# Optimization experiments

Hardware: AMD Instinct MI355X
Metric: run time of the kernel (lower is better)

## Reference

```python
import jax, jax.numpy as jnp
import numpy as np

B, LQ, LM, D, H = 2, 2048, 2048, 1024, 16
DH = D // H  # 64

def setup_inputs() -> dict:
    key = jax.random.key(0)
    ks = jax.random.split(key, 11)
    s = 0.02
    return {
        "query": jax.random.normal(ks[0], (B, LQ, D), jnp.float32),
        "memory": jax.random.normal(ks[1], (B, LM, D), jnp.float32),
        "memory_bias": jax.random.normal(ks[2], (B, LM), jnp.float32),
        "Wq": jax.random.normal(ks[3], (D, D), jnp.float32) * s,
        "bq": jnp.zeros((D,), jnp.float32),
        "Wk": jax.random.normal(ks[4], (D, D), jnp.float32) * s,
        "bk": jnp.zeros((D,), jnp.float32),
        "Wv": jax.random.normal(ks[5], (D, D), jnp.float32) * s,
        "bv": jnp.zeros((D,), jnp.float32),
        "Wo": jax.random.normal(ks[6], (D, D), jnp.float32) * s,
        "bo": jnp.zeros((D,), jnp.float32),
    }

def reference(query, memory, memory_bias, Wq, bq, Wk, bk, Wv, bv, Wo, bo):
    # QKV projections, split into heads: [B, L, H, DH]
    q = (query @ Wq + bq).reshape(B, LQ, H, DH)
    k = (memory @ Wk + bk).reshape(B, LM, H, DH)
    v = (memory @ Wv + bv).reshape(B, LM, H, DH)
    q = q * (DH ** -0.5)
    # logits: [B, H, Lq, Lk] (matches torch.einsum('btnh,bfnh->bnft', k, q))
    logits = jnp.einsum("bfnh,btnh->bnft", q, k)
    logits = logits + memory_bias[:, None, None, :]  # bias [B, Lm] -> [B,1,1,Lk]
    weights = jax.nn.softmax(logits, axis=-1)
    # dropout omitted (eval / rate 0 for correctness baseline)
    attn = jnp.einsum("bnft,btnh->bfnh", weights, v).reshape(B, LQ, D)
    return attn @ Wo + bo  # [B, Lq, output_depth]
```

## Files before the change

### kernel.cpp

```cpp
#include <hip/hip_runtime.h>
#include <hip/hip_bf16.h>
#include <math.h>


typedef __bf16 bf16;
typedef __bf16 bf16x4 __attribute__((ext_vector_type(4)));
typedef __bf16 bf16x8 __attribute__((ext_vector_type(8)));
typedef float f32x4 __attribute__((ext_vector_type(4)));

#define MFMA16(a, b, c) __builtin_amdgcn_mfma_f32_16x16x32_bf16((a), (b), (c), 0, 0, 0)

__device__ inline float exp2_hw(float x) {
    float r; asm("v_exp_f32 %0, %1" : "=v"(r) : "v"(x)); return r;
}

__device__ inline void gload_lds16(const bf16* g, bf16* l) {
    __builtin_amdgcn_global_load_lds(
        (const __attribute__((address_space(1))) void*)g,
        (__attribute__((address_space(3))) void*)l, 16, 0, 0);
}

__global__ __launch_bounds__(256) void cvt_kernel(
    const float* __restrict__ X0, const float* __restrict__ X1,
    bf16* __restrict__ Y0, bf16* __restrict__ Y1)
{
    const float* X = blockIdx.y ? X1 : X0;
    bf16* Y = blockIdx.y ? Y1 : Y0;
    const size_t i = ((size_t)blockIdx.x * 256 + threadIdx.x) * 8;
    float4 f0 = *(const float4*)&X[i];
    float4 f1 = *(const float4*)&X[i + 4];
    bf16x8 h;
    h[0] = (bf16)f0.x; h[1] = (bf16)f0.y; h[2] = (bf16)f0.z; h[3] = (bf16)f0.w;
    h[4] = (bf16)f1.x; h[5] = (bf16)f1.y; h[6] = (bf16)f1.z; h[7] = (bf16)f1.w;
    *(bf16x8*)&Y[i] = h;
}

__global__ __launch_bounds__(256) void transpose_cvt_kernel(
    const float* __restrict__ W0, const float* __restrict__ W1,
    const float* __restrict__ W2, const float* __restrict__ W3,
    bf16* __restrict__ T0, bf16* __restrict__ T1,
    bf16* __restrict__ T2, bf16* __restrict__ T3)
{
    __shared__ float Ls[64][65];
    const float* W; bf16* T;
    switch (blockIdx.z) {
        case 0:  W = W0; T = T0; break;
        case 1:  W = W1; T = T1; break;
        case 2:  W = W2; T = T2; break;
        default: W = W3; T = T3; break;
    }
    const int t = threadIdx.x;
    const int n0 = blockIdx.x * 64, k0 = blockIdx.y * 64;
    const int g = t >> 4, c = (t & 15) * 4;

    #pragma unroll
    for (int p = 0; p < 4; ++p) {
        const int row = p * 16 + g;
        float4 f = *(const float4*)&W[(size_t)(k0 + row) * 1024 + n0 + c];
        Ls[row][c + 0] = f.x; Ls[row][c + 1] = f.y;
        Ls[row][c + 2] = f.z; Ls[row][c + 3] = f.w;
    }
    __syncthreads();
    #pragma unroll
    for (int p = 0; p < 4; ++p) {
        const int n = p * 16 + g;
        bf16x4 h;
        h[0] = (bf16)Ls[c + 0][n]; h[1] = (bf16)Ls[c + 1][n];
        h[2] = (bf16)Ls[c + 2][n]; h[3] = (bf16)Ls[c + 3][n];
        *(bf16x4*)&T[(size_t)(n0 + n) * 1024 + k0 + c] = h;
    }
}

template <typename TO>
__global__ __launch_bounds__(256) void gemm_kernel(
    const bf16* __restrict__ A, const bf16* __restrict__ WT,
    const float* __restrict__ bias, TO* __restrict__ out,
    float alpha, int mode)
{
    __shared__ __align__(16) bf16 As[2][128 * 64];
    __shared__ __align__(16) bf16 Bs[2][64 * 64];

    const int fid = blockIdx.x + (blockIdx.y << 4);
    const int swz = (fid & 7) * 64 + (fid >> 3);
    const int n0 = (swz & 15) * 64;
    const int m0 = (swz >> 4) * 128;

    const int tid = threadIdx.x;
    const int w = tid >> 6, lane = tid & 63;
    const int lr = lane & 15, lg = lane >> 4;
    const int wm = (w >> 1) * 64, wn = (w & 1) * 32;

    const int arow0 = w * 32 + (lane >> 3);
    const int brow0 = w * 16 + (lane >> 3);
    const int sch = lane & 7;

    f32x4 acc[4][2] = {};

    auto stageG = [&](int kt, int bi) {
        #pragma unroll
        for (int p = 0; p < 4; ++p) {
            const int row = arow0 + p * 8;
            const int xc = ((sch ^ (row & 7)) << 3);
            gload_lds16(&A[(size_t)(m0 + row) * 1024 + kt + xc],
                        &As[bi][row * 64 + sch * 8]);
        }
        #pragma unroll
        for (int p = 0; p < 2; ++p) {
            const int row = brow0 + p * 8;
            const int xc = ((sch ^ (row & 7)) << 3);
            gload_lds16(&WT[(size_t)(n0 + row) * 1024 + kt + xc],
                        &Bs[bi][row * 64 + sch * 8]);
        }
    };

    stageG(0, 0);
    __syncthreads();

    int cur = 0;
    #pragma unroll 1
    for (int t = 0; t < 16; ++t) {
        if (t < 15) stageG((t + 1) * 64, cur ^ 1);

        #pragma unroll
        for (int ks = 0; ks < 2; ++ks) {
            const int c = (((ks * 4 + lg) ^ (lr & 7)) << 3);
            bf16x8 af[4], bfv[2];
            #pragma unroll
            for (int mt = 0; mt < 4; ++mt)
                af[mt] = *(const bf16x8*)&As[cur][(wm + mt * 16 + lr) * 64 + c];
            #pragma unroll
            for (int nt = 0; nt < 2; ++nt)
                bfv[nt] = *(const bf16x8*)&Bs[cur][(wn + nt * 16 + lr) * 64 + c];
            #pragma unroll
            for (int nt = 0; nt < 2; ++nt)
                #pragma unroll
                for (int mt = 0; mt < 4; ++mt)
                    acc[mt][nt] = MFMA16(af[mt], bfv[nt], acc[mt][nt]);
        }
        __syncthreads();
        cur ^= 1;
    }

    #pragma unroll
    for (int nt = 0; nt < 2; ++nt) {
        const int n = n0 + wn + nt * 16 + lr;
        const float bv = bias[n];
        #pragma unroll
        for (int mt = 0; mt < 4; ++mt) {
            #pragma unroll
            for (int i = 0; i < 4; ++i) {
                const int m = m0 + wm + mt * 16 + lg * 4 + i;
                const float v = (acc[mt][nt][i] + bv) * alpha;
                if (mode == 0) {
                    out[(size_t)m * 1024 + n] = (TO)v;
                } else {
                    const int b = m >> 11, t2 = m & 2047;
                    out[((size_t)(b << 10) + n) * 2048 + t2] = (TO)v;
                }
            }
        }
    }
}

__global__ __launch_bounds__(256) void gemm_kv_kernel(
    const bf16* __restrict__ A, const bf16* __restrict__ WTk,
    const bf16* __restrict__ WTv, const float* __restrict__ bk,
    const float* __restrict__ bv, bf16* __restrict__ Kout,
    bf16* __restrict__ Vtout)
{
    __shared__ __align__(16) bf16 As[2][128 * 64];
    __shared__ __align__(16) bf16 Bk[2][64 * 64];
    __shared__ __align__(16) bf16 Bv[2][64 * 64];

    const int fid = blockIdx.x + (blockIdx.y << 4);
    const int swz = (fid & 7) * 64 + (fid >> 3);
    const int n0 = (swz & 15) * 64;
    const int m0 = (swz >> 4) * 128;

    const int tid = threadIdx.x;
    const int w = tid >> 6, lane = tid & 63;
    const int lr = lane & 15, lg = lane >> 4;
    const int wm = (w >> 1) * 64, wn = (w & 1) * 32;

    const int arow0 = w * 32 + (lane >> 3);
    const int brow0 = w * 16 + (lane >> 3);
    const int sch = lane & 7;

    f32x4 accK[4][2] = {}, accV[4][2] = {};

    auto stageG = [&](int kt, int bi) {
        #pragma unroll
        for (int p = 0; p < 4; ++p) {
            const int row = arow0 + p * 8;
            const int xc = ((sch ^ (row & 7)) << 3);
            gload_lds16(&A[(size_t)(m0 + row) * 1024 + kt + xc],
                        &As[bi][row * 64 + sch * 8]);
        }
        #pragma unroll
        for (int p = 0; p < 2; ++p) {
            const int row = brow0 + p * 8;
            const int xc = ((sch ^ (row & 7)) << 3);
            gload_lds16(&WTk[(size_t)(n0 + row) * 1024 + kt + xc],
                        &Bk[bi][row * 64 + sch * 8]);
            gload_lds16(&WTv[(size_t)(n0 + row) * 1024 + kt + xc],
                        &Bv[bi][row * 64 + sch * 8]);
        }
    };

    stageG(0, 0);
    __syncthreads();

    int cur = 0;
    #pragma unroll 1
    for (int t = 0; t < 16; ++t) {
        if (t < 15) stageG((t + 1) * 64, cur ^ 1);

        #pragma unroll
        for (int ks = 0; ks < 2; ++ks) {
            const int c = (((ks * 4 + lg) ^ (lr & 7)) << 3);
            bf16x8 af[4], bkf[2], bvf[2];
            #pragma unroll
            for (int mt = 0; mt < 4; ++mt)
                af[mt] = *(const bf16x8*)&As[cur][(wm + mt * 16 + lr) * 64 + c];
            #pragma unroll
            for (int nt = 0; nt < 2; ++nt) {
                bkf[nt] = *(const bf16x8*)&Bk[cur][(wn + nt * 16 + lr) * 64 + c];
                bvf[nt] = *(const bf16x8*)&Bv[cur][(wn + nt * 16 + lr) * 64 + c];
            }
            #pragma unroll
            for (int nt = 0; nt < 2; ++nt)
                #pragma unroll
                for (int mt = 0; mt < 4; ++mt) {
                    accK[mt][nt] = MFMA16(af[mt], bkf[nt], accK[mt][nt]);
                    accV[mt][nt] = MFMA16(af[mt], bvf[nt], accV[mt][nt]);
                }
        }
        __syncthreads();
        cur ^= 1;
    }

    #pragma unroll
    for (int nt = 0; nt < 2; ++nt) {
        const int n = n0 + wn + nt * 16 + lr;
        const float bkv = bk[n], bvv = bv[n];
        #pragma unroll
        for (int mt = 0; mt < 4; ++mt) {
            #pragma unroll
            for (int i = 0; i < 4; ++i) {
                const int m = m0 + wm + mt * 16 + lg * 4 + i;
                Kout[(size_t)m * 1024 + n] = (bf16)(accK[mt][nt][i] + bkv);
                const int b = m >> 11, t2 = m & 2047;
                Vtout[((size_t)(b << 10) + n) * 2048 + t2] = (bf16)(accV[mt][nt][i] + bvv);
            }
        }
    }
}

__global__ __launch_bounds__(512, 4) void attn_kernel(
    const bf16* __restrict__ Q, const bf16* __restrict__ K,
    const bf16* __restrict__ Vt, const float* __restrict__ mbias,
    bf16* __restrict__ Oout)
{
    __shared__ __align__(16) bf16 Kbuf[4][4096];
    __shared__ __align__(16) bf16 Vbuf[4][4096];

    const int tid = threadIdx.x;
    const int w = tid >> 6, lane = tid & 63;
    const int lr = lane & 15, lg = lane >> 4;

    const int fid = blockIdx.x + (blockIdx.y << 4) + (blockIdx.z << 8);
    const int swz = (fid & 7) * 64 + (fid >> 3);
    const int qt = swz & 15, head = (swz >> 4) & 15, b = swz >> 8;
    const int qrow = qt * 128 + w * 16;

    const size_t qo = (size_t)(b * 2048 + qrow + lr) * 1024 + head * 64;
    bf16x8 qf[2];
    qf[0] = *(const bf16x8*)&Q[qo + lg * 8];
    qf[1] = *(const bf16x8*)&Q[qo + 32 + lg * 8];

    const bf16* Kb = K + (size_t)b * 2048 * 1024 + head * 64;
    const bf16* Vb = Vt + ((size_t)b * 1024 + head * 64) * 2048;
    const float* biasb = mbias + b * 2048;

    float m_run = -INFINITY;
    f32x4 of[4] = {};
    f32x4 ofl = {};

    bf16x8 ones8;
    #pragma unroll
    for (int j = 0; j < 8; ++j) ones8[j] = (bf16)1.0f;

    const int chunk = w * 64 + lane;
    const int R = chunk >> 3, cc = chunk & 7;
    const int cs = cc ^ (R & 7);
    const int piR = ((R & 16) << 1) | ((R & 12) << 1) | ((R & 32) >> 3) | (R & 3);
    auto stage = [&](int t, int slot) {
        gload_lds16(Kb + (size_t)(t * 64 + piR) * 1024 + cs * 8,
                    &Kbuf[slot][chunk * 8]);
        gload_lds16(Vb + (size_t)R * 2048 + t * 64 + cs * 8,
                    &Vbuf[slot][chunk * 8]);
    };

    stage(0, 0);
    stage(1, 1);

    const float L2E = 1.44269504f;
    f32x4 b4[4];
    b4[0] = *(const f32x4*)&biasb[8 * lg];
    b4[1] = *(const f32x4*)&biasb[32 + 8 * lg];
    b4[2] = *(const f32x4*)&biasb[4 + 8 * lg];
    b4[3] = *(const f32x4*)&biasb[36 + 8 * lg];
    #pragma unroll
    for (int nt = 0; nt < 4; ++nt) b4[nt] *= L2E;

    #pragma unroll 1
    for (int it = 0; it < 32; ++it) {
        const int slot = it & 3;
        const int tn = (it < 30) ? it + 2 : 31;
        stage(tn, (it + 2) & 3);
        asm volatile("s_waitcnt vmcnt(4)" ::: "memory");
        __builtin_amdgcn_s_barrier();
        __builtin_amdgcn_sched_barrier(0);

        f32x4 s[4];
        #pragma unroll
        for (int nt = 0; nt < 4; ++nt) s[nt] = b4[nt];
        #pragma unroll
        for (int ks = 0; ks < 2; ++ks) {
            const int cw = (((ks * 4 + lg) ^ (lr & 7)) << 3);
            bf16x8 kf[4];
            #pragma unroll
            for (int nt = 0; nt < 4; ++nt)
                kf[nt] = *(const bf16x8*)&Kbuf[slot][(nt * 16 + lr) * 64 + cw];
            __builtin_amdgcn_s_setprio(1);
            #pragma unroll
            for (int nt = 0; nt < 4; ++nt)
                s[nt] = MFMA16(kf[nt], qf[ks], s[nt]);
            __builtin_amdgcn_s_setprio(0);
        }

        const int bt = (it < 31) ? (it + 1) * 64 : 31 * 64;
        f32x4 b4n[4];
        b4n[0] = *(const f32x4*)&biasb[bt + 8 * lg];
        b4n[1] = *(const f32x4*)&biasb[bt + 32 + 8 * lg];
        b4n[2] = *(const f32x4*)&biasb[bt + 4 + 8 * lg];
        b4n[3] = *(const f32x4*)&biasb[bt + 36 + 8 * lg];

        float rml = s[0][0];
        #pragma unroll
        for (int nt = 0; nt < 4; ++nt)
            #pragma unroll
            for (int i = 0; i < 4; ++i) rml = fmaxf(rml, s[nt][i]);

        if (__any(rml > m_run + 8.f)) {
            float mx = fmaxf(rml, __shfl_xor(rml, 16, 64));
            mx = fmaxf(mx, __shfl_xor(mx, 32, 64));
            const float mnew = fmaxf(m_run, mx);
            const float al = exp2_hw(m_run - mnew);
            m_run = mnew;
            ofl *= al;
            #pragma unroll
            for (int dt = 0; dt < 4; ++dt) of[dt] *= al;
        }

        bf16x8 pb0, pb1;
        #pragma unroll
        for (int i = 0; i < 4; ++i) {
            pb0[i]     = (bf16)exp2_hw(s[0][i] - m_run);
            pb1[i]     = (bf16)exp2_hw(s[1][i] - m_run);
            pb0[4 + i] = (bf16)exp2_hw(s[2][i] - m_run);
            pb1[4 + i] = (bf16)exp2_hw(s[3][i] - m_run);
        }

        __builtin_amdgcn_s_setprio(1);
        #pragma unroll
        for (int ks = 0; ks < 2; ++ks) {
            const int cw = (((ks * 4 + lg) ^ (lr & 7)) << 3);
            const bf16x8 pb = ks ? pb1 : pb0;
            bf16x8 vf[4];
            #pragma unroll
            for (int dt = 0; dt < 4; ++dt)
                vf[dt] = *(const bf16x8*)&Vbuf[slot][(dt * 16 + lr) * 64 + cw];
            #pragma unroll
            for (int dt = 0; dt < 4; ++dt)
                of[dt] = MFMA16(vf[dt], pb, of[dt]);
            ofl = MFMA16(ones8, pb, ofl);
        }
        __builtin_amdgcn_s_setprio(0);

        #pragma unroll
        for (int nt = 0; nt < 4; ++nt) b4[nt] = b4n[nt] * L2E;
    }

    const float inv = 1.0f / ofl[0];
    const size_t ob = (size_t)(b * 2048 + qrow + lr) * 1024 + head * 64;
    #pragma unroll
    for (int dt = 0; dt < 4; ++dt) {
        bf16x4 h4;
        #pragma unroll
        for (int i = 0; i < 4; ++i) h4[i] = (bf16)(of[dt][i] * inv);
        *(bf16x4*)&Oout[ob + dt * 16 + lg * 4] = h4;
    }
}

extern "C" void kernel_launch(void* const* d_in, const int* in_sizes, int n_in,
                              void* d_out, int out_size, void* d_ws, size_t ws_size,
                              hipStream_t stream) {
    const float* query  = (const float*)d_in[0];
    const float* memory = (const float*)d_in[1];
    const float* mbias  = (const float*)d_in[2];
    const float* Wq = (const float*)d_in[3];
    const float* bq = (const float*)d_in[4];
    const float* Wk = (const float*)d_in[5];
    const float* bk = (const float*)d_in[6];
    const float* Wv = (const float*)d_in[7];
    const float* bv = (const float*)d_in[8];
    const float* Wo = (const float*)d_in[9];
    const float* bo = (const float*)d_in[10];
    float* out = (float*)d_out;

    const size_t SZ = 4096ull * 1024ull * sizeof(bf16);
    const size_t WZ = 1024ull * 1024ull * sizeof(bf16);
    char* ws = (char*)d_ws;
    bf16* Qp  = (bf16*)(ws);
    bf16* Kp  = (bf16*)(ws + SZ);
    bf16* Vtp = (bf16*)(ws + 2 * SZ);
    bf16* Ap  = (bf16*)(ws + 3 * SZ);
    bf16* WTq = (bf16*)(ws + 4 * SZ);
    bf16* WTk = (bf16*)(ws + 4 * SZ + WZ);
    bf16* WTv = (bf16*)(ws + 4 * SZ + 2 * WZ);
    bf16* WTo = (bf16*)(ws + 4 * SZ + 3 * WZ);

    dim3 blk(256);
    cvt_kernel<<<dim3(2048, 2), blk, 0, stream>>>(query, memory, Kp, Ap);
    transpose_cvt_kernel<<<dim3(16, 16, 4), blk, 0, stream>>>(
        Wq, Wk, Wv, Wo, WTq, WTk, WTv, WTo);

    dim3 gg(16, 32);
    gemm_kernel<bf16><<<gg, blk, 0, stream>>>(Kp, WTq, bq, Qp, 0.18033688f, 0);
    gemm_kv_kernel<<<gg, blk, 0, stream>>>(Ap, WTk, WTv, bk, bv, Kp, Vtp);
    attn_kernel<<<dim3(16, 16, 2), dim3(512), 0, stream>>>(Qp, Kp, Vtp, mbias, Ap);
    gemm_kernel<float><<<gg, blk, 0, stream>>>(Ap, WTo, bo, out, 1.0f, 0);
}
```

Measured before the change: 125.0 us.

## Merge prep kernels, prescale bias, and give each attention wave two query tiles

The input conversion and weight transpose kernels are fused into one prep launch, which also writes a log2e-prescaled copy of the memory bias to workspace. The attention kernel moves from 512 to 256 threads per block. Each wave now handles 32 query rows as two 16-row groups, so every K/V fragment read from LDS feeds twice as many MFMAs. The cost is more registers per wave and fewer waves to hide latency, plus many prep blocks that exit immediately.

```diff
diff --git a/kernel.cpp b/kernel.cpp
--- a/kernel.cpp
+++ b/kernel.cpp
@@ -20,39 +20,49 @@
         (__attribute__((address_space(3))) void*)l, 16, 0, 0);
 }
 
-__global__ __launch_bounds__(256) void cvt_kernel(
-    const float* __restrict__ X0, const float* __restrict__ X1,
-    bf16* __restrict__ Y0, bf16* __restrict__ Y1)
-{
-    const float* X = blockIdx.y ? X1 : X0;
-    bf16* Y = blockIdx.y ? Y1 : Y0;
-    const size_t i = ((size_t)blockIdx.x * 256 + threadIdx.x) * 8;
-    float4 f0 = *(const float4*)&X[i];
-    float4 f1 = *(const float4*)&X[i + 4];
-    bf16x8 h;
-    h[0] = (bf16)f0.x; h[1] = (bf16)f0.y; h[2] = (bf16)f0.z; h[3] = (bf16)f0.w;
-    h[4] = (bf16)f1.x; h[5] = (bf16)f1.y; h[6] = (bf16)f1.z; h[7] = (bf16)f1.w;
-    *(bf16x8*)&Y[i] = h;
-}
-
-__global__ __launch_bounds__(256) void transpose_cvt_kernel(
+__global__ __launch_bounds__(256) void prep_kernel(
+    const float* __restrict__ query, const float* __restrict__ memory,
+    const float* __restrict__ mbias,
     const float* __restrict__ W0, const float* __restrict__ W1,
     const float* __restrict__ W2, const float* __restrict__ W3,
+    bf16* __restrict__ Yq, bf16* __restrict__ Ym, float* __restrict__ sbias,
     bf16* __restrict__ T0, bf16* __restrict__ T1,
     bf16* __restrict__ T2, bf16* __restrict__ T3)
 {
     __shared__ float Ls[64][65];
+    const int t = threadIdx.x;
+
+    if (blockIdx.z == 0) {
+        const float* X = blockIdx.y ? memory : query;
+        bf16* Y = blockIdx.y ? Ym : Yq;
+        const size_t i = ((size_t)blockIdx.x * 256 + t) * 8;
+        float4 f0 = *(const float4*)&X[i];
+        float4 f1 = *(const float4*)&X[i + 4];
+        bf16x8 h;
+        h[0] = (bf16)f0.x; h[1] = (bf16)f0.y; h[2] = (bf16)f0.z; h[3] = (bf16)f0.w;
+        h[4] = (bf16)f1.x; h[5] = (bf16)f1.y; h[6] = (bf16)f1.z; h[7] = (bf16)f1.w;
+        *(bf16x8*)&Y[i] = h;
+        return;
+    }
+    const int x = blockIdx.x;
+    if (x == 1024) {
+        const int i = blockIdx.y * 2048 + t * 8;
+        #pragma unroll
+        for (int j = 0; j < 8; ++j) sbias[i + j] = mbias[i + j] * 1.44269504f;
+        return;
+    }
+    if (x > 1024 || blockIdx.y) return;
+
+    const int wsel = x >> 8, sub = x & 255;
     const float* W; bf16* T;
-    switch (blockIdx.z) {
+    switch (wsel) {
         case 0:  W = W0; T = T0; break;
         case 1:  W = W1; T = T1; break;
         case 2:  W = W2; T = T2; break;
         default: W = W3; T = T3; break;
     }
-    const int t = threadIdx.x;
-    const int n0 = blockIdx.x * 64, k0 = blockIdx.y * 64;
+    const int n0 = (sub & 15) * 64, k0 = (sub >> 4) * 64;
     const int g = t >> 4, c = (t & 15) * 4;
-
     #pragma unroll
     for (int p = 0; p < 4; ++p) {
         const int row = p * 16 + g;
@@ -256,9 +266,9 @@
     }
 }
 
-__global__ __launch_bounds__(512, 4) void attn_kernel(
+__global__ __launch_bounds__(256) void attn_kernel(
     const bf16* __restrict__ Q, const bf16* __restrict__ K,
-    const bf16* __restrict__ Vt, const float* __restrict__ mbias,
+    const bf16* __restrict__ Vt, const float* __restrict__ sbias,
     bf16* __restrict__ Oout)
 {
     __shared__ __align__(16) bf16 Kbuf[4][4096];
@@ -271,60 +281,66 @@
     const int fid = blockIdx.x + (blockIdx.y << 4) + (blockIdx.z << 8);
     const int swz = (fid & 7) * 64 + (fid >> 3);
     const int qt = swz & 15, head = (swz >> 4) & 15, b = swz >> 8;
-    const int qrow = qt * 128 + w * 16;
-
-    const size_t qo = (size_t)(b * 2048 + qrow + lr) * 1024 + head * 64;
-    bf16x8 qf[2];
-    qf[0] = *(const bf16x8*)&Q[qo + lg * 8];
-    qf[1] = *(const bf16x8*)&Q[qo + 32 + lg * 8];
+    const int qrow = qt * 128 + w * 32;
+
+    bf16x8 qf[2][2];
+    #pragma unroll
+    for (int g = 0; g < 2; ++g) {
+        const size_t qo = (size_t)(b * 2048 + qrow + g * 16 + lr) * 1024 + head * 64;
+        qf[g][0] = *(const bf16x8*)&Q[qo + lg * 8];
+        qf[g][1] = *(const bf16x8*)&Q[qo + 32 + lg * 8];
+    }
 
     const bf16* Kb = K + (size_t)b * 2048 * 1024 + head * 64;
     const bf16* Vb = Vt + ((size_t)b * 1024 + head * 64) * 2048;
-    const float* biasb = mbias + b * 2048;
-
-    float m_run = -INFINITY;
-    f32x4 of[4] = {};
-    f32x4 ofl = {};
+    const float* biasb = sbias + b * 2048;
+
+    float m_run[2] = {-INFINITY, -INFINITY};
+    f32x4 of[2][4] = {};
+    f32x4 ofl[2] = {};
 
     bf16x8 ones8;
     #pragma unroll
     for (int j = 0; j < 8; ++j) ones8[j] = (bf16)1.0f;
 
-    const int chunk = w * 64 + lane;
-    const int R = chunk >> 3, cc = chunk & 7;
-    const int cs = cc ^ (R & 7);
-    const int piR = ((R & 16) << 1) | ((R & 12) << 1) | ((R & 32) >> 3) | (R & 3);
     auto stage = [&](int t, int slot) {
-        gload_lds16(Kb + (size_t)(t * 64 + piR) * 1024 + cs * 8,
-                    &Kbuf[slot][chunk * 8]);
-        gload_lds16(Vb + (size_t)R * 2048 + t * 64 + cs * 8,
-                    &Vbuf[slot][chunk * 8]);
+        #pragma unroll
+        for (int cp = 0; cp < 2; ++cp) {
+            const int chunk = cp * 256 + tid;
+            const int R = chunk >> 3, cc = chunk & 7;
+            const int cs = cc ^ (R & 7);
+            const int piR = ((R & 16) << 1) | ((R & 12) << 1) | ((R & 32) >> 3) | (R & 3);
+            gload_lds16(Kb + (size_t)(t * 64 + piR) * 1024 + cs * 8,
+                        &Kbuf[slot][chunk * 8]);
+            gload_lds16(Vb + (size_t)R * 2048 + t * 64 + cs * 8,
+                        &Vbuf[slot][chunk * 8]);
+        }
     };
 
     stage(0, 0);
     stage(1, 1);
-
-    const float L2E = 1.44269504f;
-    f32x4 b4[4];
-    b4[0] = *(const f32x4*)&biasb[8 * lg];
-    b4[1] = *(const f32x4*)&biasb[32 + 8 * lg];
-    b4[2] = *(const f32x4*)&biasb[4 + 8 * lg];
-    b4[3] = *(const f32x4*)&biasb[36 + 8 * lg];
-    #pragma unroll
-    for (int nt = 0; nt < 4; ++nt) b4[nt] *= L2E;
 
     #pragma unroll 1
     for (int it = 0; it < 32; ++it) {
         const int slot = it & 3;
         const int tn = (it < 30) ? it + 2 : 31;
         stage(tn, (it + 2) & 3);
-        asm volatile("s_waitcnt vmcnt(4)" ::: "memory");
+        asm volatile("s_waitcnt vmcnt(8)" ::: "memory");
         __builtin_amdgcn_s_barrier();
         __builtin_amdgcn_sched_barrier(0);
 
-        f32x4 s[4];
-        #pragma unroll
-        for (int nt = 0; nt < 4; ++nt) s[nt] = b4[nt];
+        const int bt = it * 64;
+        f32x4 b4[4];
+        b4[0] = *(const f32x4*)&biasb[bt + 8 * lg];
+        b4[1] = *(const f32x4*)&biasb[bt + 32 + 8 * lg];
+        b4[2] = *(const f32x4*)&biasb[bt + 4 + 8 * lg];
+        b4[3] = *(const f32x4*)&biasb[bt + 36 + 8 * lg];
+
+        f32x4 s[2][4];
+        #pragma unroll
+        for (int g = 0; g < 2; ++g)
+            #pragma unroll
+            for (int nt = 0; nt < 4; ++nt) s[g][nt] = b4[nt];
         #pragma unroll
         for (int ks = 0; ks < 2; ++ks) {
             const int cw = (((ks * 4 + lg) ^ (lr & 7)) << 3);
@@ -334,72 +350,79 @@
                 kf[nt] = *(const bf16x8*)&Kbuf[slot][(nt * 16 + lr) * 64 + cw];
             __builtin_amdgcn_s_setprio(1);
             #pragma unroll
-            for (int nt = 0; nt < 4; ++nt)
-                s[nt] = MFMA16(kf[nt], qf[ks], s[nt]);
+            for (int nt = 0; nt < 4; ++nt) {
+                s[0][nt] = MFMA16(kf[nt], qf[0][ks], s[0][nt]);
+                s[1][nt] = MFMA16(kf[nt], qf[1][ks], s[1][nt]);
+            }
             __builtin_amdgcn_s_setprio(0);
         }
 
-        const int bt = (it < 31) ? (it + 1) * 64 : 31 * 64;
-        f32x4 b4n[4];
-        b4n[0] = *(const f32x4*)&biasb[bt + 8 * lg];
-        b4n[1] = *(const f32x4*)&biasb[bt + 32 + 8 * lg];
-        b4n[2] = *(const f32x4*)&biasb[bt + 4 + 8 * lg];
-        b4n[3] = *(const f32x4*)&biasb[bt + 36 + 8 * lg];
-
-        float rml = s[0][0];
-        #pragma unroll
-        for (int nt = 0; nt < 4; ++nt)
-            #pragma unroll
-            for (int i = 0; i < 4; ++i) rml = fmaxf(rml, s[nt][i]);
-
-        if (__any(rml > m_run + 8.f)) {
-            float mx = fmaxf(rml, __shfl_xor(rml, 16, 64));
-            mx = fmaxf(mx, __shfl_xor(mx, 32, 64));
-            const float mnew = fmaxf(m_run, mx);
-            const float al = exp2_hw(m_run - mnew);
-            m_run = mnew;
-            ofl *= al;
-            #pragma unroll
-            for (int dt = 0; dt < 4; ++dt) of[dt] *= al;
-        }
-
-        bf16x8 pb0, pb1;
-        #pragma unroll
-        for (int i = 0; i < 4; ++i) {
-            pb0[i]     = (bf16)exp2_hw(s[0][i] - m_run);
-            pb1[i]     = (bf16)exp2_hw(s[1][i] - m_run);
-            pb0[4 + i] = (bf16)exp2_hw(s[2][i] - m_run);
-            pb1[4 + i] = (bf16)exp2_hw(s[3][i] - m_run);
-        }
+        float rml[2];
+        #pragma unroll
+        for (int g = 0; g < 2; ++g) {
+            float m0 = fmaxf(fmaxf(s[g][0][0], s[g][0][1]), fmaxf(s[g][0][2], s[g][0][3]));
+            float m1 = fmaxf(fmaxf(s[g][1][0], s[g][1][1]), fmaxf(s[g][1][2], s[g][1][3]));
+            float m2 = fmaxf(fmaxf(s[g][2][0], s[g][2][1]), fmaxf(s[g][2][2], s[g][2][3]));
+            float m3 = fmaxf(fmaxf(s[g][3][0], s[g][3][1]), fmaxf(s[g][3][2], s[g][3][3]));
+            rml[g] = fmaxf(fmaxf(m0, m1), fmaxf(m2, m3));
+        }
+        const bool need = (rml[0] > m_run[0] + 8.f) || (rml[1] > m_run[1] + 8.f);
+
+        if (__any(need)) {
+            #pragma unroll
+            for (int g = 0; g < 2; ++g) {
+                float mx = fmaxf(rml[g], __shfl_xor(rml[g], 16, 64));
+                mx = fmaxf(mx, __shfl_xor(mx, 32, 64));
+                const float mnew = fmaxf(m_run[g], mx);
+                const float al = exp2_hw(m_run[g] - mnew);
+                m_run[g] = mnew;
+                ofl[g] *= al;
+                #pragma unroll
+                for (int dt = 0; dt < 4; ++dt) of[g][dt] *= al;
+            }
+        }
+
+        bf16x8 pb[2][2];
+        #pragma unroll
+        for (int g = 0; g < 2; ++g)
+            #pragma unroll
+            for (int i = 0; i < 4; ++i) {
+                pb[g][0][i]     = (bf16)exp2_hw(s[g][0][i] - m_run[g]);
+                pb[g][1][i]     = (bf16)exp2_hw(s[g][1][i] - m_run[g]);
+                pb[g][0][4 + i] = (bf16)exp2_hw(s[g][2][i] - m_run[g]);
+                pb[g][1][4 + i] = (bf16)exp2_hw(s[g][3][i] - m_run[g]);
+            }
 
         __builtin_amdgcn_s_setprio(1);
         #pragma unroll
         for (int ks = 0; ks < 2; ++ks) {
             const int cw = (((ks * 4 + lg) ^ (lr & 7)) << 3);
-            const bf16x8 pb = ks ? pb1 : pb0;
             bf16x8 vf[4];
             #pragma unroll
             for (int dt = 0; dt < 4; ++dt)
                 vf[dt] = *(const bf16x8*)&Vbuf[slot][(dt * 16 + lr) * 64 + cw];
             #pragma unroll
-            for (int dt = 0; dt < 4; ++dt)
-                of[dt] = MFMA16(vf[dt], pb, of[dt]);
-            ofl = MFMA16(ones8, pb, ofl);
+            for (int g = 0; g < 2; ++g) {
+                #pragma unroll
+                for (int dt = 0; dt < 4; ++dt)
+                    of[g][dt] = MFMA16(vf[dt], pb[g][ks], of[g][dt]);
+                ofl[g] = MFMA16(ones8, pb[g][ks], ofl[g]);
+            }
         }
         __builtin_amdgcn_s_setprio(0);
-
-        #pragma unroll
-        for (int nt = 0; nt < 4; ++nt) b4[nt] = b4n[nt] * L2E;
-    }
-
-    const float inv = 1.0f / ofl[0];
-    const size_t ob = (size_t)(b * 2048 + qrow + lr) * 1024 + head * 64;
-    #pragma unroll
-    for (int dt = 0; dt < 4; ++dt) {
-        bf16x4 h4;
-        #pragma unroll
-        for (int i = 0; i < 4; ++i) h4[i] = (bf16)(of[dt][i] * inv);
-        *(bf16x4*)&Oout[ob + dt * 16 + lg * 4] = h4;
+    }
+
+    #pragma unroll
+    for (int g = 0; g < 2; ++g) {
+        const float inv = 1.0f / ofl[g][0];
+        const size_t ob = (size_t)(b * 2048 + qrow + g * 16 + lr) * 1024 + head * 64;
+        #pragma unroll
+        for (int dt = 0; dt < 4; ++dt) {
+            bf16x4 h4;
+            #pragma unroll
+            for (int i = 0; i < 4; ++i) h4[i] = (bf16)(of[g][dt][i] * inv);
+            *(bf16x4*)&Oout[ob + dt * 16 + lg * 4] = h4;
+        }
     }
 }
 
@@ -430,15 +453,15 @@
     bf16* WTk = (bf16*)(ws + 4 * SZ + WZ);
     bf16* WTv = (bf16*)(ws + 4 * SZ + 2 * WZ);
     bf16* WTo = (bf16*)(ws + 4 * SZ + 3 * WZ);
+    float* sbias = (float*)(ws + 4 * SZ + 4 * WZ);
 
     dim3 blk(256);
-    cvt_kernel<<<dim3(2048, 2), blk, 0, stream>>>(query, memory, Kp, Ap);
-    transpose_cvt_kernel<<<dim3(16, 16, 4), blk, 0, stream>>>(
-        Wq, Wk, Wv, Wo, WTq, WTk, WTv, WTo);
+    prep_kernel<<<dim3(2048, 2, 2), blk, 0, stream>>>(
+        query, memory, mbias, Wq, Wk, Wv, Wo, Kp, Ap, sbias, WTq, WTk, WTv, WTo);
 
     dim3 gg(16, 32);
     gemm_kernel<bf16><<<gg, blk, 0, stream>>>(Kp, WTq, bq, Qp, 0.18033688f, 0);
     gemm_kv_kernel<<<gg, blk, 0, stream>>>(Ap, WTk, WTv, bk, bv, Kp, Vtp);
-    attn_kernel<<<dim3(16, 16, 2), dim3(512), 0, stream>>>(Qp, Kp, Vtp, mbias, Ap);
+    attn_kernel<<<dim3(16, 16, 2), blk, 0, stream>>>(Qp, Kp, Vtp, sbias, Ap);
     gemm_kernel<float><<<gg, blk, 0, stream>>>(Ap, WTo, bo, out, 1.0f, 0);
 }
```

New measurement: 129.3 us. 1.03x slower.
